# Optimization experiments

Hardware: AMD Instinct MI355X
Metric: run time of the kernel (lower is better)

The kernel has to match this reference:

```python
import jax, jax.numpy as jnp
import numpy as np

D = 1024

def setup_inputs() -> dict:
    key = jax.random.key(0)
    ks = jax.random.split(key, 9)
    s = 1.0 / np.sqrt(D)
    x = jax.random.normal(ks[0], (4096, 8, D), dtype=jnp.float32)
    Wq = jax.random.uniform(ks[1], (D, D), jnp.float32, -s, s)
    bq = jax.random.uniform(ks[2], (D,), jnp.float32, -s, s)
    Wk = jax.random.uniform(ks[3], (D, D), jnp.float32, -s, s)
    bk = jax.random.uniform(ks[4], (D,), jnp.float32, -s, s)
    Wv = jax.random.uniform(ks[5], (D, D), jnp.float32, -s, s)
    bv = jax.random.uniform(ks[6], (D,), jnp.float32, -s, s)
    Wo = jax.random.uniform(ks[7], (D, D), jnp.float32, -s, s)
    bo = jax.random.uniform(ks[8], (D,), jnp.float32, -s, s)
    return {"x": x, "Wq": Wq, "bq": bq, "Wk": Wk, "bk": bk,
            "Wv": Wv, "bv": bv, "Wo": Wo, "bo": bo}

def reference(x, Wq, bq, Wk, bk, Wv, bv, Wo, bo):
    # x: (S, B, D) seq-first, matching torch module
    Q = jax.nn.elu(x @ Wq.T + bq) + 1.0  # (S,B,D)
    K = jax.nn.elu(x @ Wk.T + bk) + 1.0  # (S,B,D)
    V = x @ Wv.T + bv                    # (S,B,D)
    # KV = K^T V per batch: (B, D, D)
    KV = jnp.einsum('sbd,sbe->bde', K, V)
    # out = Q @ KV per batch, back to (S,B,D)
    out = jnp.einsum('sbd,bde->sbe', Q, KV)
    return out @ Wo.T + bo
```

## Files before the change

### kernel.cpp

```cpp
#include <hip/hip_runtime.h>


typedef __bf16 bf16;
typedef __attribute__((ext_vector_type(8))) __bf16 bf16x8;
typedef __attribute__((ext_vector_type(4))) __bf16 bf16x4;
typedef __attribute__((ext_vector_type(4))) float f32x4;

static constexpr int S = 4096;
static constexpr int B = 8;
static constexpr int D = 1024;
static constexpr int SB = S * B;
static constexpr long long NELEM = (long long)SB * D;

__device__ __forceinline__ void load_lds16(const bf16* g, void* l)
{
    __builtin_amdgcn_global_load_lds(
        (const __attribute__((address_space(1))) void*)g,
        (__attribute__((address_space(3))) void*)l, 16, 0, 0);
}

__global__ void cvt_w3(const float* __restrict__ w0, const float* __restrict__ w1,
                       const float* __restrict__ w2, bf16* __restrict__ o0,
                       bf16* __restrict__ o1, bf16* __restrict__ o2)
{
    const float* in;
    bf16* out;
    if (blockIdx.y == 0)      { in = w0; out = o0; }
    else if (blockIdx.y == 1) { in = w1; out = o1; }
    else                      { in = w2; out = o2; }
    int i = (blockIdx.x * blockDim.x + threadIdx.x) * 4;
    float4 v = *(const float4*)(in + i);
    bf16x4 o;
    o[0] = (bf16)v.x; o[1] = (bf16)v.y; o[2] = (bf16)v.z; o[3] = (bf16)v.w;
    *(bf16x4*)(out + i) = o;
}

__global__ void cvt_permute(const float* __restrict__ in, bf16* __restrict__ out)
{
    long long i = ((long long)blockIdx.x * blockDim.x + threadIdx.x) * 8;
    const long long stride = (long long)gridDim.x * blockDim.x * 8;
    for (; i < NELEM; i += stride) {
        const long long s = i >> 13;
        const long long r = i & 8191;
        const long long b = r >> 10;
        const long long d = r & 1023;
        float4 v0 = *(const float4*)(in + i);
        float4 v1 = *(const float4*)(in + i + 4);
        bf16x8 o;
        o[0] = (bf16)v0.x; o[1] = (bf16)v0.y; o[2] = (bf16)v0.z; o[3] = (bf16)v0.w;
        o[4] = (bf16)v1.x; o[5] = (bf16)v1.y; o[6] = (bf16)v1.z; o[7] = (bf16)v1.w;
        *(bf16x8*)(out + b * ((long long)S * D) + s * D + d) = o;
    }
}

__global__ __launch_bounds__(256) void transpose_bsd_bds(
    const bf16* __restrict__ in, bf16* __restrict__ out)
{
    __shared__ bf16 tile[64 * 72];
    const int b  = blockIdx.z;
    const int s0 = blockIdx.x * 64;
    const int f0 = blockIdx.y * 64;
    const int t  = threadIdx.x;
    const int rl = t >> 3;
    const int c8 = (t & 7) * 8;
    const long long SD = (long long)S * D;

    #pragma unroll
    for (int p = 0; p < 2; ++p) {
        int r = rl + p * 32;
        bf16x8 v = *(const bf16x8*)(in + b * SD + (long long)(s0 + r) * D + f0 + c8);
        #pragma unroll
        for (int j = 0; j < 8; ++j)
            tile[(c8 + j) * 72 + r] = v[j];
    }
    __syncthreads();
    #pragma unroll
    for (int p = 0; p < 2; ++p) {
        int fr = rl + p * 32;
        *(bf16x8*)(out + b * SD + (long long)(f0 + fr) * S + s0 + c8) =
            *(const bf16x8*)(&tile[fr * 72 + c8]);
    }
}

__global__ __launch_bounds__(256) void cvt_transpose_1024(
    const float* __restrict__ in, bf16* __restrict__ out)
{
    __shared__ bf16 tile[64][72];
    const int e0 = blockIdx.y * 64;
    const int d0 = blockIdx.x * 64;
    const int t  = threadIdx.x;
    const int rl = t >> 3;
    const int c8 = (t & 7) * 8;
    #pragma unroll
    for (int p = 0; p < 2; ++p) {
        int r = rl + p * 32;
        float4 v0 = *(const float4*)(in + (long long)(e0 + r) * D + d0 + c8);
        float4 v1 = *(const float4*)(in + (long long)(e0 + r) * D + d0 + c8 + 4);
        tile[c8+0][r] = (bf16)v0.x; tile[c8+1][r] = (bf16)v0.y;
        tile[c8+2][r] = (bf16)v0.z; tile[c8+3][r] = (bf16)v0.w;
        tile[c8+4][r] = (bf16)v1.x; tile[c8+5][r] = (bf16)v1.y;
        tile[c8+6][r] = (bf16)v1.z; tile[c8+7][r] = (bf16)v1.w;
    }
    __syncthreads();
    #pragma unroll
    for (int p = 0; p < 2; ++p) {
        int dr = rl + p * 32;
        *(bf16x8*)(out + (long long)(d0 + dr) * D + e0 + c8) = *(bf16x8*)(&tile[dr][c8]);
    }
}

__global__ __launch_bounds__(256) void bvo_kernel(
    const float* __restrict__ Wo, const float* __restrict__ bv, float* __restrict__ bvo)
{
    const int row = blockIdx.x;
    const int t = threadIdx.x;
    float4 w = *(const float4*)(Wo + (long long)row * D + t * 4);
    float4 b = *(const float4*)(bv + t * 4);
    float s = w.x*b.x + w.y*b.y + w.z*b.z + w.w*b.w;
    __shared__ float red[256];
    red[t] = s; __syncthreads();
    for (int off = 128; off > 0; off >>= 1) {
        if (t < off) red[t] += red[t + off];
        __syncthreads();
    }
    if (t == 0) bvo[row] = red[0];
}

__global__ __launch_bounds__(256) void kcolsum(const bf16* __restrict__ Kt,
                                               float* __restrict__ ks)
{
    const int row  = blockIdx.x * 4 + (threadIdx.x >> 6);
    const int lane = threadIdx.x & 63;
    const bf16* r = Kt + (long long)row * S;
    float s = 0.0f;
    #pragma unroll
    for (int it = 0; it < 8; ++it) {
        bf16x8 v = *(const bf16x8*)(r + it * 512 + lane * 8);
        #pragma unroll
        for (int j = 0; j < 8; ++j) s += (float)v[j];
    }
    #pragma unroll
    for (int off = 32; off > 0; off >>= 1) s += __shfl_down(s, off);
    if (lane == 0) ks[row] = s;
}

__global__ __launch_bounds__(256) void kv_add(bf16* __restrict__ p)
{
    const long long DD = (long long)D * D;
    const int b = blockIdx.y;
    const long long i = ((long long)blockIdx.x * 256 + threadIdx.x) * 8;
    bf16x8 u = *(const bf16x8*)(p + (2 * b) * DD + i);
    bf16x8 v = *(const bf16x8*)(p + (2 * b + 1) * DD + i);
    bf16x8 r;
    #pragma unroll
    for (int j = 0; j < 8; ++j) r[j] = (bf16)((float)u[j] + (float)v[j]);
    *(bf16x8*)(p + (2 * b) * DD + i) = r;
}

template<int BM, int BN, int WM, int WN, int EPI, int OUTF32, int BIASROW>
__global__ __launch_bounds__(WM * WN * 64, 2) void gemm_bt(
    const bf16* __restrict__ A, const bf16* __restrict__ Bm,
    const float* __restrict__ bias, void* __restrict__ Cout,
    int lda, int ldb, int ldc, int K,
    long long aBatch, long long bBatch, long long cBatch)
{
    constexpr int THREADS = WM * WN * 64;
    constexpr int WROWS = BM / WM, WCOLS = BN / WN;
    constexpr int MI = WROWS / 16, NI = WCOLS / 16;
    constexpr int ABYTES = BM * 64;
    constexpr int BBYTES = BN * 64;
    constexpr int BUF = ABYTES + BBYTES;

    __shared__ unsigned char smem[4 * BUF];

    const int tid  = threadIdx.x;
    const int lane = tid & 63;
    const int wave = tid >> 6;
    const int wr   = wave / WN;
    const int wc   = wave % WN;
    const int bz   = blockIdx.z;

    const int nx  = gridDim.x;
    const int bid = blockIdx.y * nx + blockIdx.x;
    const int cpx = (nx * gridDim.y) >> 3;
    const int swz = (bid & 7) * cpx + (bid >> 3);
    const long long m0 = (long long)(swz / nx) * BM;
    const long long n0 = (long long)(swz % nx) * BN;

    const bf16* Ab = A  + bz * aBatch + m0 * lda;
    const bf16* Bb = Bm + bz * bBatch + n0 * ldb;

    f32x4 acc[MI][NI] = {};
    const int NT = K >> 5;

    auto stage = [&](int t) {
        unsigned char* dst = smem + (t & 3) * BUF;
        const long long kk = (long long)t << 5;
        #pragma unroll
        for (int j = 0; j < 2; ++j) {
            const int g  = wave * 64 + lane + j * THREADS;
            const int gs = g ^ ((g >> 3) & 3);
            const int row = gs >> 2, col = (gs & 3) * 8;
            load_lds16(Ab + (long long)row * lda + kk + col,
                       dst + (wave * 64 + j * THREADS) * 16);
        }
        #pragma unroll
        for (int j = 0; j < 2; ++j) {
            const int g  = wave * 64 + lane + j * THREADS;
            const int gs = g ^ ((g >> 3) & 3);
            const int row = gs >> 2, col = (gs & 3) * 8;
            load_lds16(Bb + (long long)row * ldb + kk + col,
                       dst + ABYTES + (wave * 64 + j * THREADS) * 16);
        }
    };

    stage(0); stage(1); stage(2);

    const int ko2 = (lane >> 4) * 16;
    const int la15 = lane & 15;

    for (int t = 0; t < NT; ++t) {
        if (t + 2 < NT)      asm volatile("s_waitcnt vmcnt(8)" ::: "memory");
        else if (t + 1 < NT) asm volatile("s_waitcnt vmcnt(4)" ::: "memory");
        else                 asm volatile("s_waitcnt vmcnt(0)" ::: "memory");
        __builtin_amdgcn_s_barrier();
        asm volatile("" ::: "memory");

        if (t + 3 < NT) stage(t + 3);

        const unsigned char* buf = smem + (t & 3) * BUF;
        bf16x8 a[MI], b[NI];
        #pragma unroll
        for (int mi = 0; mi < MI; ++mi) {
            int ad = (wr * WROWS + mi * 16 + la15) * 64 + ko2;
            ad ^= ((ad >> 7) & 3) << 4;
            a[mi] = *(const bf16x8*)(buf + ad);
        }
        #pragma unroll
        for (int ni = 0; ni < NI; ++ni) {
            int ad = (wc * WCOLS + ni * 16 + la15) * 64 + ko2;
            ad ^= ((ad >> 7) & 3) << 4;
            b[ni] = *(const bf16x8*)(buf + ABYTES + ad);
        }

        __builtin_amdgcn_s_setprio(1);
        #pragma unroll
        for (int mi = 0; mi < MI; ++mi)
            #pragma unroll
            for (int ni = 0; ni < NI; ++ni)
                acc[mi][ni] = __builtin_amdgcn_mfma_f32_16x16x32_bf16(
                    a[mi], b[ni], acc[mi][ni], 0, 0, 0);
        __builtin_amdgcn_s_setprio(0);
    }

    const int crow = (lane >> 4) * 4;
    const int ccol = lane & 15;
    #pragma unroll
    for (int ni = 0; ni < NI; ++ni) {
        const long long c = n0 + wc * WCOLS + ni * 16 + ccol;
        float bcol = 0.0f;
        if (!BIASROW && bias) bcol = bias[c];
        #pragma unroll
        for (int mi = 0; mi < MI; ++mi) {
            const long long r0 = m0 + wr * WROWS + mi * 16 + crow;
            #pragma unroll
            for (int j = 0; j < 4; ++j) {
                float v = acc[mi][ni][j];
                v += BIASROW ? bias[r0 + j] : bcol;
                if (EPI == 1) v = (v > 0.0f) ? (v + 1.0f) : __expf(v);
                const long long idx = bz * cBatch + (r0 + j) * ldc + c;
                if (OUTF32) ((float*)Cout)[idx] = v;
                else        ((bf16*)Cout)[idx]  = (bf16)v;
            }
        }
    }
}

template<int EPI, int OUTF32, int BIASROW, int SPLITK, int GROUPN>
__global__ __launch_bounds__(512, 1) void gemm8p(
    const bf16* __restrict__ A, const bf16* __restrict__ Bm,
    const float* __restrict__ bias, const float* __restrict__ ksum,
    void* __restrict__ Cout,
    int lda, int ldb, int ldc, int K,
    long long aBatch, long long bBatch, long long cBatch)
{
    __shared__ unsigned char smem[131072];

    const int tid  = threadIdx.x;
    const int lane = tid & 63;
    const int wave = tid >> 6;
    const int wr   = wave >> 2;
    const int wc   = wave & 3;
    const int bz    = blockIdx.z;
    const int batch = bz / SPLITK;
    const int kseg  = bz % SPLITK;

    const int nx  = gridDim.x;
    const int ny  = gridDim.y;
    const int bid = blockIdx.y * nx + blockIdx.x;
    const int cpx = (nx * ny) >> 3;
    const int swzb = (bid & 7) * cpx + (bid >> 3);
    long long m0, n0;
    if (GROUPN) { n0 = (long long)(swzb / ny) * 256; m0 = (long long)(swzb % ny) * 256; }
    else        { m0 = (long long)(swzb / nx) * 256; n0 = (long long)(swzb % nx) * 256; }

    const bf16* Ab = A  + batch * aBatch + m0 * lda + (long long)kseg * K;
    const bf16* Bb = Bm + batch * bBatch + n0 * ldb + (long long)kseg * K;

    const int sg = (lane & 3) ^ ((lane >> 3) & 3);
    const long long srow = wave * 32 + (lane >> 2);
    const bf16* srcA  = Ab + srow * lda + sg * 8;
    const bf16* srcA2 = srcA + 16 * (long long)lda;
    const bf16* srcB  = Bb + srow * ldb + sg * 8;
    const bf16* srcB2 = srcB + 16 * (long long)ldb;
    const int dstoff = wave * 2048;

    const int la15 = lane & 15;
    const int rsw  = (lane >> 4) ^ ((la15 >> 1) & 3);
    const int a16  = (wr * 128 + la15) * 4 + rsw;
    const int b16  = (wc * 64  + la15) * 4 + rsw;

    f32x4 acc[8][4] = {};
    const int NT = K >> 6;
    const int NI = NT >> 1;

    auto stageA = [&](int T, int kh) {
        const int reg = ((((T & 1) << 1) | kh) << 14);
        const long long kp = ((long long)T << 6) + (kh << 5);
        load_lds16(srcA  + kp, smem + reg + dstoff);
        load_lds16(srcA2 + kp, smem + reg + dstoff + 1024);
    };
    auto stageB = [&](int T, int kh) {
        const int reg = 65536 + ((((T & 1) << 1) | kh) << 14);
        const long long kp = ((long long)T << 6) + (kh << 5);
        load_lds16(srcB  + kp, smem + reg + dstoff);
        load_lds16(srcB2 + kp, smem + reg + dstoff + 1024);
    };

    stageB(0, 0); stageA(0, 0); stageB(0, 1); stageA(0, 1);
    stageB(1, 0); stageA(1, 0); stageB(1, 1);
    asm volatile("s_waitcnt vmcnt(6)" ::: "memory");

    bf16x8 bfr[4];
    for (int i = 0; i < NI; ++i) {
        const int t = 2 * i;
        const bool nl = (i + 1 < NI);
        #pragma unroll
        for (int p = 0; p < 8; ++p) {
            const int ks  = (p >> 1) & 1;
            const int ch  = p & 1;
            const int buf = p >> 2;
            const int regA = ((buf << 1) | ks) << 14;
            const int regB = 65536 + regA;

            __builtin_amdgcn_s_barrier();
            __builtin_amdgcn_sched_barrier(0);

            bf16x8 afr[4];
            if (ch == 0) {
                #pragma unroll
                for (int ni = 0; ni < 4; ++ni)
                    bfr[ni] = *(const bf16x8*)(smem + regB + (b16 + ni * 64) * 16);
            }
            #pragma unroll
            for (int m4 = 0; m4 < 4; ++m4)
                afr[m4] = *(const bf16x8*)(smem + regA + (a16 + (ch * 4 + m4) * 64) * 16);

            if      (p == 0) stageA(t + 1, 1);
            else if (p == 1) { if (t + 2 < NT) stageB(t + 2, 0); }
            else if (p == 2) { if (t + 2 < NT) stageA(t + 2, 0); }
            else if (p == 3) { if (t + 2 < NT) stageB(t + 2, 1); }
            else if (p == 4) { if (t + 2 < NT) stageA(t + 2, 1); }
            else if (p == 5) { if (t + 3 < NT) stageB(t + 3, 0); }
            else if (p == 6) { if (t + 3 < NT) stageA(t + 3, 0); }
            else             { if (t + 3 < NT) stageB(t + 3, 1); }

            if (p == 3) {
                if (nl) asm volatile("s_waitcnt vmcnt(6)" ::: "memory");
                else    asm volatile("s_waitcnt vmcnt(0)" ::: "memory");
            } else if (p == 7) {
                if (nl) asm volatile("s_waitcnt vmcnt(6)" ::: "memory");
            }

            __builtin_amdgcn_s_setprio(1);
            #pragma unroll
            for (int m4 = 0; m4 < 4; ++m4)
                #pragma unroll
                for (int ni = 0; ni < 4; ++ni)
                    acc[ch * 4 + m4][ni] = __builtin_amdgcn_mfma_f32_16x16x32_bf16(
                        afr[m4], bfr[ni], acc[ch * 4 + m4][ni], 0, 0, 0);
            __builtin_amdgcn_s_setprio(0);
        }
    }

    const bool doElu = (EPI == 1) || (EPI == 2 && m0 < 1024);
    const long long cb = (long long)bz * cBatch;
    const int crow = (lane >> 4) * 4;

    if constexpr (OUTF32 != 0) {
        float* lt = (float*)smem;
        #pragma unroll
        for (int q = 0; q < 4; ++q) {
            __builtin_amdgcn_s_barrier();
            __builtin_amdgcn_sched_barrier(0);
            if (wr == (q >> 1)) {
                #pragma unroll
                for (int m4 = 0; m4 < 4; ++m4) {
                    const int mi = (q & 1) * 4 + m4;
                    const int lrow = m4 * 16 + crow;
                    const long long r0 = m0 + q * 64 + lrow;
                    #pragma unroll
                    for (int ni = 0; ni < 4; ++ni) {
                        const int lcol = wc * 64 + ni * 16 + la15;
                        float bb = 0.0f;
                        if (!BIASROW && bias) bb = bias[n0 + lcol];
                        #pragma unroll
                        for (int j = 0; j < 4; ++j) {
                            float v = acc[mi][ni][j] + (BIASROW ? bias[r0 + j] : bb);
                            if (doElu) v = (v > 0.0f) ? (v + 1.0f) : __expf(v);
                            lt[(lrow + j) * 260 + lcol] = v;
                        }
                    }
                }
            }
            __builtin_amdgcn_s_barrier();
            #pragma unroll
            for (int it = 0; it < 8; ++it) {
                const int chk = it * 512 + tid;
                const int r   = chk >> 6;
                const int g   = chk & 63;
                float4 v = *(const float4*)(lt + r * 260 + g * 4);
                *(float4*)((float*)Cout + cb + (m0 + q * 64 + r) * ldc + n0 + g * 4) = v;
            }
        }
    } else {
        bf16* lt = (bf16*)smem;
        #pragma unroll
        for (int half = 0; half < 2; ++half) {
            __builtin_amdgcn_s_barrier();
            __builtin_amdgcn_sched_barrier(0);
            if (wr == half) {
                #pragma unroll
                for (int mi = 0; mi < 8; ++mi) {
                    const int lrow = mi * 16 + crow;
                    const long long r0 = m0 + half * 128 + lrow;
                    #pragma unroll
                    for (int ni = 0; ni < 4; ++ni) {
                        const int lcol = wc * 64 + ni * 16 + la15;
                        float bb = 0.0f;
                        if (!BIASROW && bias) bb = bias[n0 + lcol];
                        float ksv = 0.0f;
                        if (EPI == 3 && ksum)
                            ksv = ksum[(long long)batch * D + n0 + lcol];
                        #pragma unroll
                        for (int j = 0; j < 4; ++j) {
                            float v;
                            if (EPI == 3) {
                                v = acc[mi][ni][j] + bias[r0 + j] * ksv;
                            } else {
                                v = acc[mi][ni][j] + (BIASROW ? bias[r0 + j] : bb);
                                if (doElu) v = (v > 0.0f) ? (v + 1.0f) : __expf(v);
                            }
                            lt[(lrow + j) * 264 + lcol] = (bf16)v;
                        }
                    }
                }
            }
            __builtin_amdgcn_s_barrier();
            #pragma unroll
            for (int it = 0; it < 8; ++it) {
                const int chk = it * 512 + tid;
                const int m   = chk >> 5;
                const int nof = (chk & 31) * 8;
                bf16x8 v = *(const bf16x8*)(lt + m * 264 + nof);
                *(bf16x8*)((bf16*)Cout + cb + (m0 + half * 128 + m) * ldc + n0 + nof) = v;
            }
        }
    }
}

extern "C" void kernel_launch(void* const* d_in, const int* in_sizes, int n_in,
                              void* d_out, int out_size, void* d_ws, size_t ws_size,
                              hipStream_t stream)
{
    const float* x  = (const float*)d_in[0];
    const float* Wq = (const float*)d_in[1];
    const float* bq = (const float*)d_in[2];
    const float* Wk = (const float*)d_in[3];
    const float* bk = (const float*)d_in[4];
    const float* Wv = (const float*)d_in[5];
    const float* bv = (const float*)d_in[6];
    const float* Wo = (const float*)d_in[7];
    const float* bo = (const float*)d_in[8];
    float* out = (float*)d_out;

    char* ws = (char*)d_ws;
    if (ws_size < (size_t)159383552) return;
    bf16*  xbp  = (bf16*)(ws + 0);
    bf16*  part = (bf16*)(ws + 67108864);
    bf16*  Qb   = (bf16*)(ws + 67108864);
    float* ks   = (float*)(ws + 100663296);
    float* bvo  = (float*)(ws + 100663296 + 32768);
    bf16*  wvT  = (bf16*)(ws + 134217728);
    bf16*  KVo  = (bf16*)(ws + 134217728);
    bf16*  wqb  = (bf16*)(ws + 150994944);
    bf16*  wob  = wqb + 1048576;
    bf16*  wkb  = wob + 1048576;
    bf16*  Wvo  = wkb + 1048576;
    bf16*  Kt   = (bf16*)d_out;
    bf16*  xT   = Kt + NELEM;

    const long long SD = (long long)S * D;
    const long long DD = (long long)D * D;

    cvt_permute<<<8192, 256, 0, stream>>>(x, xbp);
    cvt_w3<<<dim3(1024, 3), 256, 0, stream>>>(Wq, Wo, Wk, wqb, wob, wkb);
    cvt_transpose_1024<<<dim3(16, 16), 256, 0, stream>>>(Wv, wvT);
    bvo_kernel<<<1024, 256, 0, stream>>>(Wo, bv, bvo);
    transpose_bsd_bds<<<dim3(64, 16, 8), 256, 0, stream>>>(xbp, xT);

    gemm_bt<128, 128, 2, 2, 0, 0, 0><<<dim3(8, 8, 1), 256, 0, stream>>>(
        wob, wvT, nullptr, Wvo, D, D, D, D, 0, 0, 0);

    gemm8p<1, 0, 1, 1, 1><<<dim3(16, 4, 8), 512, 0, stream>>>(
        wkb, xbp, bk, nullptr, Kt, D, D, S, D, 0, SD, SD);

    kcolsum<<<2048, 256, 0, stream>>>(Kt, ks);

    gemm8p<0, 0, 0, 2, 0><<<dim3(4, 4, 16), 512, 0, stream>>>(
        Kt, xT, nullptr, nullptr, part, S, S, D, 2048, SD, SD, DD);

    kv_add<<<dim3(512, 8), 256, 0, stream>>>(part);

    gemm8p<3, 0, 1, 1, 0><<<dim3(4, 4, 8), 512, 0, stream>>>(
        Wvo, part, bvo, ks, KVo, D, D, D, D, 0, 2 * DD, DD);

    gemm8p<1, 0, 0, 1, 0><<<dim3(4, 16, 8), 512, 0, stream>>>(
        xbp, wqb, bq, nullptr, Qb, D, D, D, D, SD, 0, SD);

    gemm8p<0, 1, 0, 1, 0><<<dim3(4, 16, 8), 512, 0, stream>>>(
        Qb, KVo, bo, nullptr, out, D, D, B * D, D,
        SD, DD, (long long)D);
}
```

Baseline: 467.5 us.

## Fuse x permute with transpose and K column-sum into K GEMM epilogue

Merges the fp32→bf16 permute and the bsd→bds transpose into one kernel, so x is read once and both layouts are written from the same tile. The separate kcolsum pass over Kt is removed: the K-projection GEMM epilogue now sums each row from the LDS output tile and adds it into ks with atomics, after ks is zeroed with a memset. This drops one full read of the bf16 x copy, one full read of Kt and two launches. In exchange it adds atomics and an extra memset, and the float atomic accumulation order is nondeterministic.

```diff
diff --git a/kernel.cpp b/kernel.cpp
--- a/kernel.cpp
+++ b/kernel.cpp
@@ -35,26 +35,8 @@
     *(bf16x4*)(out + i) = o;
 }
 
-__global__ void cvt_permute(const float* __restrict__ in, bf16* __restrict__ out)
-{
-    long long i = ((long long)blockIdx.x * blockDim.x + threadIdx.x) * 8;
-    const long long stride = (long long)gridDim.x * blockDim.x * 8;
-    for (; i < NELEM; i += stride) {
-        const long long s = i >> 13;
-        const long long r = i & 8191;
-        const long long b = r >> 10;
-        const long long d = r & 1023;
-        float4 v0 = *(const float4*)(in + i);
-        float4 v1 = *(const float4*)(in + i + 4);
-        bf16x8 o;
-        o[0] = (bf16)v0.x; o[1] = (bf16)v0.y; o[2] = (bf16)v0.z; o[3] = (bf16)v0.w;
-        o[4] = (bf16)v1.x; o[5] = (bf16)v1.y; o[6] = (bf16)v1.z; o[7] = (bf16)v1.w;
-        *(bf16x8*)(out + b * ((long long)S * D) + s * D + d) = o;
-    }
-}
-
-__global__ __launch_bounds__(256) void transpose_bsd_bds(
-    const bf16* __restrict__ in, bf16* __restrict__ out)
+__global__ __launch_bounds__(256) void cvt_permute_both(
+    const float* __restrict__ in, bf16* __restrict__ xbp, bf16* __restrict__ xT)
 {
     __shared__ bf16 tile[64 * 72];
     const int b  = blockIdx.z;
@@ -67,17 +49,23 @@
 
     #pragma unroll
     for (int p = 0; p < 2; ++p) {
-        int r = rl + p * 32;
-        bf16x8 v = *(const bf16x8*)(in + b * SD + (long long)(s0 + r) * D + f0 + c8);
+        const int r = rl + p * 32;
+        const float* src = in + (long long)(s0 + r) * (B * D) + b * D + f0 + c8;
+        float4 v0 = *(const float4*)(src);
+        float4 v1 = *(const float4*)(src + 4);
+        bf16x8 o;
+        o[0] = (bf16)v0.x; o[1] = (bf16)v0.y; o[2] = (bf16)v0.z; o[3] = (bf16)v0.w;
+        o[4] = (bf16)v1.x; o[5] = (bf16)v1.y; o[6] = (bf16)v1.z; o[7] = (bf16)v1.w;
+        *(bf16x8*)(xbp + b * SD + (long long)(s0 + r) * D + f0 + c8) = o;
         #pragma unroll
         for (int j = 0; j < 8; ++j)
-            tile[(c8 + j) * 72 + r] = v[j];
+            tile[(c8 + j) * 72 + r] = o[j];
     }
     __syncthreads();
     #pragma unroll
     for (int p = 0; p < 2; ++p) {
-        int fr = rl + p * 32;
-        *(bf16x8*)(out + b * SD + (long long)(f0 + fr) * S + s0 + c8) =
+        const int fr = rl + p * 32;
+        *(bf16x8*)(xT + b * SD + (long long)(f0 + fr) * S + s0 + c8) =
             *(const bf16x8*)(&tile[fr * 72 + c8]);
     }
 }
@@ -126,24 +114,6 @@
     if (t == 0) bvo[row] = red[0];
 }
 
-__global__ __launch_bounds__(256) void kcolsum(const bf16* __restrict__ Kt,
-                                               float* __restrict__ ks)
-{
-    const int row  = blockIdx.x * 4 + (threadIdx.x >> 6);
-    const int lane = threadIdx.x & 63;
-    const bf16* r = Kt + (long long)row * S;
-    float s = 0.0f;
-    #pragma unroll
-    for (int it = 0; it < 8; ++it) {
-        bf16x8 v = *(const bf16x8*)(r + it * 512 + lane * 8);
-        #pragma unroll
-        for (int j = 0; j < 8; ++j) s += (float)v[j];
-    }
-    #pragma unroll
-    for (int off = 32; off > 0; off >>= 1) s += __shfl_down(s, off);
-    if (lane == 0) ks[row] = s;
-}
-
 __global__ __launch_bounds__(256) void kv_add(bf16* __restrict__ p)
 {
     const long long DD = (long long)D * D;
@@ -279,7 +249,7 @@
 template<int EPI, int OUTF32, int BIASROW, int SPLITK, int GROUPN>
 __global__ __launch_bounds__(512, 1) void gemm8p(
     const bf16* __restrict__ A, const bf16* __restrict__ Bm,
-    const float* __restrict__ bias, const float* __restrict__ ksum,
+    const float* __restrict__ bias, float* __restrict__ ksum,
     void* __restrict__ Cout,
     int lda, int ldb, int ldc, int K,
     long long aBatch, long long bBatch, long long cBatch)
@@ -393,7 +363,7 @@
         }
     }
 
-    const bool doElu = (EPI == 1) || (EPI == 2 && m0 < 1024);
+    const bool doElu = (EPI == 1) || (EPI == 4) || (EPI == 2 && m0 < 1024);
     const long long cb = (long long)bz * cBatch;
     const int crow = (lane >> 4) * 4;
 
@@ -475,6 +445,23 @@
                 bf16x8 v = *(const bf16x8*)(lt + m * 264 + nof);
                 *(bf16x8*)((bf16*)Cout + cb + (m0 + half * 128 + m) * ldc + n0 + nof) = v;
             }
+            if constexpr (EPI == 4) {
+                const int row = tid >> 2;
+                const int seg = (tid & 3) * 66;
+                const bf16* rp = lt + row * 264 + (tid & 3) * 64;
+                float s = 0.0f;
+                #pragma unroll
+                for (int e8 = 0; e8 < 8; ++e8) {
+                    bf16x8 v = *(const bf16x8*)(rp + e8 * 8);
+                    #pragma unroll
+                    for (int j = 0; j < 8; ++j) s += (float)v[j];
+                }
+                (void)seg;
+                s += __shfl_down(s, 2);
+                s += __shfl_down(s, 1);
+                if ((tid & 3) == 0)
+                    atomicAdd(ksum + (long long)batch * D + m0 + half * 128 + row, s);
+            }
         }
     }
 }
@@ -513,19 +500,17 @@
     const long long SD = (long long)S * D;
     const long long DD = (long long)D * D;
 
-    cvt_permute<<<8192, 256, 0, stream>>>(x, xbp);
+    cvt_permute_both<<<dim3(64, 16, 8), 256, 0, stream>>>(x, xbp, xT);
     cvt_w3<<<dim3(1024, 3), 256, 0, stream>>>(Wq, Wo, Wk, wqb, wob, wkb);
     cvt_transpose_1024<<<dim3(16, 16), 256, 0, stream>>>(Wv, wvT);
     bvo_kernel<<<1024, 256, 0, stream>>>(Wo, bv, bvo);
-    transpose_bsd_bds<<<dim3(64, 16, 8), 256, 0, stream>>>(xbp, xT);
+    hipMemsetAsync(ks, 0, B * D * sizeof(float), stream);
 
     gemm_bt<128, 128, 2, 2, 0, 0, 0><<<dim3(8, 8, 1), 256, 0, stream>>>(
         wob, wvT, nullptr, Wvo, D, D, D, D, 0, 0, 0);
 
-    gemm8p<1, 0, 1, 1, 1><<<dim3(16, 4, 8), 512, 0, stream>>>(
-        wkb, xbp, bk, nullptr, Kt, D, D, S, D, 0, SD, SD);
-
-    kcolsum<<<2048, 256, 0, stream>>>(Kt, ks);
+    gemm8p<4, 0, 1, 1, 1><<<dim3(16, 4, 8), 512, 0, stream>>>(
+        wkb, xbp, bk, ks, Kt, D, D, S, D, 0, SD, SD);
 
     gemm8p<0, 0, 0, 2, 0><<<dim3(4, 4, 16), 512, 0, stream>>>(
         Kt, xT, nullptr, nullptr, part, S, S, D, 2048, SD, SD, DD);
```

Result: no change. 458.7 us (-1.9%).
